# Kernel tuning notes

Hardware: AMD Instinct MI355X
Metric: run time of the kernel (lower is better)

The kernel has to match this reference:

```python
import jax, jax.numpy as jnp
import numpy as np

# dims
V = 50000      # vocab_size
DW = 50        # word_embed_size
DP = 5         # pos_embed_size
D = DW + 2 * DP  # input_size = 60
OC = 230       # out_c
NREL = 53      # n_rel
POSV = 61      # 2*pos_limit + 1
LIMIT = 30     # piecewise split threshold
G, B, L = 1000, 8, 120  # n_bags, bag_size, sentence length


def setup_inputs() -> dict:
    key = jax.random.key(0)
    ks = jax.random.split(key, 11)
    f32 = jnp.float32
    words = jax.random.randint(ks[0], (G, B, L), 0, V, dtype=jnp.int32)
    pos = jax.random.randint(ks[1], (G, B, L, 2), 0, POSV, dtype=jnp.int32)
    # pretrained-style word embeddings + position embeddings
    w2v = jax.random.normal(ks[2], (V, DW), f32) * 0.1
    pos1_emb = jax.random.normal(ks[3], (POSV, DP), f32) * 0.1
    pos2_emb = jax.random.normal(ks[4], (POSV, DP), f32) * 0.1
    con1 = float(np.sqrt(6.0 / ((DP + DW) * 3)))
    conv_w = jax.random.uniform(ks[5], (OC, 1, 3, D), f32, -con1, con1)  # OIHW
    conv_b0 = jax.random.uniform(ks[6], (1, OC), f32, -con1, con1)
    conv_b1 = jax.random.uniform(ks[7], (1, OC), f32, -con1, con1)
    conv_b2 = jax.random.uniform(ks[8], (1, OC), f32, -con1, con1)
    con = float(np.sqrt(6.0 / (OC + NREL)))
    r_embed = jax.random.uniform(ks[9], (NREL, 3 * OC), f32, -con, con)
    r_bias = jax.random.uniform(ks[10], (NREL,), f32, -con, con)
    return dict(words=words, pos=pos, w2v=w2v, pos1_emb=pos1_emb,
                pos2_emb=pos2_emb, conv_w=conv_w, conv_b0=conv_b0,
                conv_b1=conv_b1, conv_b2=conv_b2, r_embed=r_embed,
                r_bias=r_bias)


def reference(words, pos, w2v, pos1_emb, pos2_emb, conv_w,
              conv_b0, conv_b1, conv_b2, r_embed, r_bias):
    g, bag, ln = words.shape
    n = g * bag
    w = words.reshape(n, ln)
    p = pos.reshape(n, ln, 2)
    # embedding lookups -> [N, L, D]
    x = jnp.concatenate([w2v[w], pos1_emb[p[..., 0]], pos2_emb[p[..., 1]]], axis=-1)
    # Conv1d(1, OC, (3, D), padding=(1, 0)) over [N,1,L,D] -> [N,OC,L]
    feat = jax.lax.conv_general_dilated(
        x[:, None, :, :], conv_w, window_strides=(1, 1),
        padding=((1, 1), (0, 0)),
        dimension_numbers=('NCHW', 'OIHW', 'NCHW'))[..., 0]
    # piecewise masks from position ids
    p1 = (p[..., 0] >= LIMIT).astype(feat.dtype)  # [N, L]
    p2 = (p[..., 1] >= LIMIT).astype(feat.dtype)
    left = p1 * p2
    right = (1.0 - p1) * (1.0 - p2)
    mid = 1.0 - left - right

    def pool(mask, bias):  # masked max over sequence + per-piece bias
        return jnp.max(feat * mask[:, None, :], axis=-1) + bias  # [N, OC]

    f = jnp.concatenate([pool(left, conv_b0), pool(mid, conv_b1),
                         pool(right, conv_b2)], axis=-1)  # [N, 3*OC]
    f = jnp.tanh(f)
    # eval mode: dropout identity, logits scaled by 0.5 before bias
    logits = (f @ r_embed.T) * 0.5 + r_bias  # [N, NREL]
    logp = jax.nn.log_softmax(logits, axis=-1).reshape(g, bag, NREL)
    # eval mode: max over sentences in each bag
    return jnp.max(logp, axis=1)  # [G, NREL]
```

## Files before the change

### kernel.cpp

```cpp
#include <hip/hip_runtime.h>
#include <hip/hip_bf16.h>
#include <math.h>

typedef __bf16 bf16;
typedef __bf16 bf16x4 __attribute__((ext_vector_type(4)));
typedef __bf16 bf16x8 __attribute__((ext_vector_type(8)));
typedef float f32x4 __attribute__((ext_vector_type(4)));

#define OCC 230
#define NRELS 53
#define W2V48_OFF 0
#define WTAIL_OFF 2400000
#define PCAT_OFF  2500000
#define REMBB_OFF 2559552
#define CONVB_OFF 2608704
#define FLWS_OFF  2657862

union FragU { bf16x8 v8; bf16x4 v4[2]; bf16 e[8]; };

__global__ void pcnn_prep(const float* __restrict__ w2v, const float* __restrict__ p1e,
                          const float* __restrict__ p2e, const float* __restrict__ remb,
                          const float* __restrict__ convw, bf16* __restrict__ wsb) {
  const int i = blockIdx.x * 256 + threadIdx.x;
  if (i < 300000) {
    const int w = i / 6, c = i - 6 * w;
    const float2* s = reinterpret_cast<const float2*>(w2v + w * 50 + c * 8);
    const float2 f0 = s[0], f1 = s[1], f2 = s[2], f3 = s[3];
    bf16x8 v = {(bf16)f0.x, (bf16)f0.y, (bf16)f1.x, (bf16)f1.y,
                (bf16)f2.x, (bf16)f2.y, (bf16)f3.x, (bf16)f3.y};
    *reinterpret_cast<bf16x8*>(wsb + W2V48_OFF + w * 48 + c * 8) = v;
    return;
  }
  int e = i - 300000;
  if (e < 50000) {
    const float2 f = *reinterpret_cast<const float2*>(w2v + e * 50 + 48);
    wsb[WTAIL_OFF + 2 * e]     = (bf16)f.x;
    wsb[WTAIL_OFF + 2 * e + 1] = (bf16)f.y;
    return;
  }
  e -= 50000;
  if (e < 7442) {
    const int row = e >> 1, h = e & 1;
    const int v1 = row / 61, v2 = row - v1 * 61;
    bf16x8 v;
    if (h == 0) {
      v[0] = (bf16)p1e[v1 * 5 + 0]; v[1] = (bf16)p1e[v1 * 5 + 1];
      v[2] = (bf16)p1e[v1 * 5 + 2]; v[3] = (bf16)p1e[v1 * 5 + 3];
      v[4] = (bf16)p1e[v1 * 5 + 4]; v[5] = (bf16)p2e[v2 * 5 + 0];
      v[6] = (bf16)0.f; v[7] = (bf16)0.f;
    } else {
      v[0] = (bf16)p2e[v2 * 5 + 1]; v[1] = (bf16)p2e[v2 * 5 + 2];
      v[2] = (bf16)p2e[v2 * 5 + 3]; v[3] = (bf16)p2e[v2 * 5 + 4];
      v[4] = (bf16)0.f; v[5] = (bf16)0.f; v[6] = (bf16)0.f; v[7] = (bf16)0.f;
    }
    *reinterpret_cast<bf16x8*>(wsb + PCAT_OFF + row * 16 + h * 8) = v;
    return;
  }
  e -= 7442;
  if (e < 6144) {
    const int r = e / 96, c0 = (e - r * 96) * 8;
    bf16x8 v;
#pragma unroll
    for (int j = 0; j < 8; ++j) {
      const int cc = c0 + j, p = cc >> 8, oc = cc & 255;
      v[j] = (r < NRELS && oc < OCC) ? (bf16)remb[r * 690 + p * OCC + oc] : (bf16)0.f;
    }
    *reinterpret_cast<bf16x8*>(wsb + REMBB_OFF + r * 768 + c0) = v;
    return;
  }
  e -= 6144;
  if (e < 6144) {
    const int oc = e / 24, k0 = (e - oc * 24) * 8;
    bf16x8 v;
#pragma unroll
    for (int j = 0; j < 8; ++j) {
      const int k = k0 + j;
      v[j] = (oc < OCC && k < 180) ? (bf16)convw[oc * 180 + k] : (bf16)0.f;
    }
    *reinterpret_cast<bf16x8*>(wsb + CONVB_OFF + oc * 192 + k0) = v;
  }
}

#define XE 7352

__global__ __launch_bounds__(256, 3)
void pcnn_conv(const int* __restrict__ words, const int* __restrict__ posi,
               const float* __restrict__ cb0, const float* __restrict__ cb1,
               const float* __restrict__ cb2, const bf16* __restrict__ wsb,
               bf16* __restrict__ flws)
{
  __shared__ __align__(16) bf16 xlds[XE];
  __shared__ int widx[120];

  const int t = threadIdx.x;
  const int bid = blockIdx.x;
  const int ns = bid >> 1;
  const int ochalf = bid & 1;
  const int wv = t >> 6, lane = t & 63, g = lane >> 4, cl = lane & 15;

  if (t < 120) {
    const int w = words[ns * 120 + t];
    const int2 pp = *reinterpret_cast<const int2*>(posi + ns * 240 + 2 * t);
    const bool b0 = pp.x >= 30, b1 = pp.y >= 30;
    const int pc = (b0 && b1) ? 0 : ((!b0 && !b1) ? 2 : 1);
    widx[t] = w | ((pp.x * 61 + pp.y) << 16) | (pc << 28);
  }
  if (t < 16) {
    const int r = (t >> 3) ? 121 : 0;
    const int gr = t & 7;
    const int eo = r * 60 + ((gr < 7) ? gr * 8 : 52);
    *reinterpret_cast<int2*>(&xlds[eo])     = int2{0, 0};
    *reinterpret_cast<int2*>(&xlds[eo + 4]) = int2{0, 0};
  }

  FragU Bf[2][6];
  {
    const bf16* cwb = wsb + CONVB_OFF;
#pragma unroll
    for (int nt = 0; nt < 2; ++nt) {
      const int oc = ochalf * 128 + wv * 32 + nt * 16 + cl;
#pragma unroll
      for (int ks = 0; ks < 6; ++ks)
        Bf[nt][ks].v8 = *reinterpret_cast<const bf16x8*>(cwb + oc * 192 + ks * 32 + g * 8);
    }
  }
  __syncthreads();

#pragma unroll
  for (int k = 0; k < 4; ++k) {
    const int gi = t + k * 256;
    if (gi < 960) {
      const int lr = 1 + (gi >> 3), gr = gi & 7;
      const int wi = widx[lr - 1];
      const int word = wi & 0xFFFF;
      const int pidx = (wi >> 16) & 0xFFF;
      if (gr < 6) {
        const int4 v = *reinterpret_cast<const int4*>(wsb + W2V48_OFF + word * 48 + gr * 8);
        bf16* d = &xlds[lr * 60 + gr * 8];
        *reinterpret_cast<int2*>(d)     = int2{v.x, v.y};
        *reinterpret_cast<int2*>(d + 4) = int2{v.z, v.w};
      } else if (gr == 6) {
        const int wt = *(reinterpret_cast<const int*>(wsb + WTAIL_OFF) + word);
        const int4 pc4 = *reinterpret_cast<const int4*>(wsb + PCAT_OFF + pidx * 16);
        bf16* d = &xlds[lr * 60 + 48];
        *reinterpret_cast<int2*>(d)     = int2{wt, pc4.x};
        *reinterpret_cast<int2*>(d + 4) = int2{pc4.y, pc4.z};
      } else {
        const int2 v = *reinterpret_cast<const int2*>(wsb + PCAT_OFF + pidx * 16 + 8);
        *reinterpret_cast<int2*>(&xlds[lr * 60 + 56]) = v;
      }
    }
  }
  __syncthreads();

  int mrow[8];
#pragma unroll
  for (int mt = 0; mt < 8; ++mt) {
    const int m = mt * 16 + cl;
    mrow[mt] = (m < 120 ? m : 119) * 60;
  }

  f32x4 acc[8][2];
  const f32x4 z4 = {0.f, 0.f, 0.f, 0.f};
#pragma unroll
  for (int mt = 0; mt < 8; ++mt) { acc[mt][0] = z4; acc[mt][1] = z4; }

#pragma unroll
  for (int ks = 0; ks < 6; ++ks) {
    const int ko = ks * 32 + g * 8;
#pragma unroll
    for (int mt = 0; mt < 8; ++mt) {
      FragU a;
      a.v4[0] = *reinterpret_cast<const bf16x4*>(&xlds[mrow[mt] + ko]);
      a.v4[1] = *reinterpret_cast<const bf16x4*>(&xlds[mrow[mt] + ko + 4]);
#pragma unroll
      for (int nt = 0; nt < 2; ++nt)
        acc[mt][nt] = __builtin_amdgcn_mfma_f32_16x16x32_bf16(
            a.v8, Bf[nt][ks].v8, acc[mt][nt], 0, 0, 0);
    }
  }

  float pool[2][3];
#pragma unroll
  for (int nt = 0; nt < 2; ++nt) { pool[nt][0] = pool[nt][1] = pool[nt][2] = -INFINITY; }
#pragma unroll
  for (int mt = 0; mt < 8; ++mt) {
    const int l0 = mt * 16 + g * 4;
    if (l0 < 120) {
      const int4 pv = *reinterpret_cast<const int4*>(&widx[l0]);
      const int pcs[4] = {(int)((unsigned)pv.x >> 28), (int)((unsigned)pv.y >> 28),
                          (int)((unsigned)pv.z >> 28), (int)((unsigned)pv.w >> 28)};
#pragma unroll
      for (int r = 0; r < 4; ++r) {
        const int p = pcs[r];
#pragma unroll
        for (int nt = 0; nt < 2; ++nt) {
          const float v = acc[mt][nt][r];
          pool[nt][0] = fmaxf(pool[nt][0], p == 0 ? v : 0.0f);
          pool[nt][1] = fmaxf(pool[nt][1], p == 1 ? v : 0.0f);
          pool[nt][2] = fmaxf(pool[nt][2], p == 2 ? v : 0.0f);
        }
      }
    }
  }
#pragma unroll
  for (int nt = 0; nt < 2; ++nt)
#pragma unroll
    for (int p = 0; p < 3; ++p) {
      float x = pool[nt][p];
      x = fmaxf(x, __shfl_xor(x, 16));
      x = fmaxf(x, __shfl_xor(x, 32));
      pool[nt][p] = x;
    }

  if (g == 0) {
#pragma unroll
    for (int nt = 0; nt < 2; ++nt) {
      const int ocg = ochalf * 128 + wv * 32 + nt * 16 + cl;
      if (ocg < OCC) {
        const float b0v = cb0[ocg], b1v = cb1[ocg], b2v = cb2[ocg];
        bf16* fr = flws + ns * 768;
        fr[ocg]       = (bf16)tanhf(pool[nt][0] + b0v);
        fr[256 + ocg] = (bf16)tanhf(pool[nt][1] + b1v);
        fr[512 + ocg] = (bf16)tanhf(pool[nt][2] + b2v);
      }
    }
  }
}

__global__ __launch_bounds__(256)
void pcnn_logits(const bf16* __restrict__ wsb, const bf16* __restrict__ flws,
                 const float* __restrict__ rbias, float* __restrict__ out)
{
  __shared__ __align__(16) bf16 fl_lds[6144];
  __shared__ float logits_l[8][64];

  const int t = threadIdx.x;
  const int bag = blockIdx.x;
  const int wv = t >> 6, lane = t & 63, g = lane >> 4, cl = lane & 15;

#pragma unroll
  for (int j = 0; j < 3; ++j) {
    const bf16* src = flws + bag * 6144 + (j * 256 + t) * 8;
    bf16* dst = &fl_lds[(j * 256 + wv * 64) * 8];
    __builtin_amdgcn_global_load_lds(
        (const __attribute__((address_space(1))) void*)src,
        (__attribute__((address_space(3))) void*)dst, 16, 0, 0);
  }
  asm volatile("s_waitcnt vmcnt(0)" ::: "memory");
  __syncthreads();

  f32x4 lac = {0.f, 0.f, 0.f, 0.f};
  const bf16* brow = wsb + REMBB_OFF + (wv * 16 + cl) * 768 + g * 8;
  const bf16x8 zf = {(bf16)0.f, (bf16)0.f, (bf16)0.f, (bf16)0.f,
                     (bf16)0.f, (bf16)0.f, (bf16)0.f, (bf16)0.f};
#pragma unroll
  for (int ks = 0; ks < 24; ++ks) {
    const bf16x8 afr = (cl < 8)
        ? *reinterpret_cast<const bf16x8*>(&fl_lds[cl * 768 + ks * 32 + g * 8]) : zf;
    const bf16x8 bfr = *reinterpret_cast<const bf16x8*>(brow + ks * 32);
    lac = __builtin_amdgcn_mfma_f32_16x16x32_bf16(afr, bfr, lac, 0, 0, 0);
  }
  if (g < 2) {
    const int rel = wv * 16 + cl;
    const float bias = (rel < NRELS) ? rbias[rel] : 0.0f;
#pragma unroll
    for (int r = 0; r < 4; ++r)
      logits_l[g * 4 + r][rel] = lac[r] * 0.5f + bias;
  }
  __syncthreads();

#pragma unroll
  for (int rep = 0; rep < 2; ++rep) {
    const int s = wv + rep * 4;
    const float x = (lane < NRELS) ? logits_l[s][lane] : -INFINITY;
    float m = x;
#pragma unroll
    for (int off = 32; off; off >>= 1) m = fmaxf(m, __shfl_xor(m, off));
    const float e = (lane < NRELS) ? __expf(x - m) : 0.0f;
    float sm = e;
#pragma unroll
    for (int off = 32; off; off >>= 1) sm += __shfl_xor(sm, off);
    if (lane < NRELS) logits_l[s][lane] = x - m - __logf(sm);
  }
  __syncthreads();

  if (t < NRELS) {
    float m = logits_l[0][t];
#pragma unroll
    for (int s2 = 1; s2 < 8; ++s2) m = fmaxf(m, logits_l[s2][t]);
    out[bag * NRELS + t] = m;
  }
}

extern "C" void kernel_launch(void* const* d_in, const int* in_sizes, int n_in,
                              void* d_out, int out_size, void* d_ws, size_t ws_size,
                              hipStream_t stream) {
  const int* words  = (const int*)d_in[0];
  const int* posi   = (const int*)d_in[1];
  const float* w2v  = (const float*)d_in[2];
  const float* p1e  = (const float*)d_in[3];
  const float* p2e  = (const float*)d_in[4];
  const float* cw   = (const float*)d_in[5];
  const float* cb0  = (const float*)d_in[6];
  const float* cb1  = (const float*)d_in[7];
  const float* cb2  = (const float*)d_in[8];
  const float* remb = (const float*)d_in[9];
  const float* rbias= (const float*)d_in[10];
  bf16* wsb = (bf16*)d_ws;
  bf16* flws = wsb + FLWS_OFF;
  float* out = (float*)d_out;

  pcnn_prep<<<1445, 256, 0, stream>>>(w2v, p1e, p2e, remb, cw, wsb);
  pcnn_conv<<<16000, 256, 0, stream>>>(words, posi, cb0, cb1, cb2, wsb, flws);
  pcnn_logits<<<1000, 256, 0, stream>>>(wsb, flws, rbias, out);
}
```

Measured before the change: 313.7 us.

## Double-buffer gathered embeddings with async global-to-LDS loads over four sentences per block

The conv kernel now runs 512-thread blocks that cover all 256 output channels and loop over four sentences. The embedding rows of the next sentence are gathered into a second LDS buffer with global_load_lds while the current one is being computed. The LDS rows are padded to a stride of 64 and XOR-swizzled, and the conv weights are re-laid out per tap, so each A fragment is one 16-byte read without bank conflicts. Conv weights and biases are loaded once per block instead of once per sentence. The trade-offs are fewer blocks (2000 instead of 16000), a larger per-block LDS footprint, and a full-buffer zeroing pass at the start of each block.

Result: slower. 342.7 us (+9.3%).

```diff
diff --git a/kernel.cpp b/kernel.cpp
--- a/kernel.cpp
+++ b/kernel.cpp
@@ -14,7 +14,7 @@
 #define PCAT_OFF  2500000
 #define REMBB_OFF 2559552
 #define CONVB_OFF 2608704
-#define FLWS_OFF  2657862
+#define FLWS_OFF  2657864
 
 union FragU { bf16x8 v8; bf16x4 v4[2]; bf16 e[8]; };
 
@@ -74,43 +74,44 @@
     bf16x8 v;
 #pragma unroll
     for (int j = 0; j < 8; ++j) {
-      const int k = k0 + j;
-      v[j] = (oc < OCC && k < 180) ? (bf16)convw[oc * 180 + k] : (bf16)0.f;
+      const int kp = k0 + j, tap = kp >> 6, d = kp & 63;
+      v[j] = (oc < OCC && d < 60) ? (bf16)convw[oc * 180 + tap * 60 + d] : (bf16)0.f;
     }
     *reinterpret_cast<bf16x8*>(wsb + CONVB_OFF + oc * 192 + k0) = v;
   }
 }
 
-#define XE 7352
-
-__global__ __launch_bounds__(256, 3)
+#define XROWS 122
+#define XSTR 64
+#define XBUFE (XROWS * XSTR)
+
+__global__ __launch_bounds__(512, 4)
 void pcnn_conv(const int* __restrict__ words, const int* __restrict__ posi,
                const float* __restrict__ cb0, const float* __restrict__ cb1,
                const float* __restrict__ cb2, const bf16* __restrict__ wsb,
                bf16* __restrict__ flws)
 {
-  __shared__ __align__(16) bf16 xlds[XE];
-  __shared__ int widx[120];
+  __shared__ __align__(16) bf16 xb[2][XBUFE];
+  __shared__ int widx[480];
 
   const int t = threadIdx.x;
-  const int bid = blockIdx.x;
-  const int ns = bid >> 1;
-  const int ochalf = bid & 1;
+  const int sb = blockIdx.x * 4;
   const int wv = t >> 6, lane = t & 63, g = lane >> 4, cl = lane & 15;
 
-  if (t < 120) {
-    const int w = words[ns * 120 + t];
-    const int2 pp = *reinterpret_cast<const int2*>(posi + ns * 240 + 2 * t);
+  if (t < 480) {
+    const int w = words[sb * 120 + t];
+    const int2 pp = *reinterpret_cast<const int2*>(posi + sb * 240 + 2 * t);
     const bool b0 = pp.x >= 30, b1 = pp.y >= 30;
     const int pc = (b0 && b1) ? 0 : ((!b0 && !b1) ? 2 : 1);
     widx[t] = w | ((pp.x * 61 + pp.y) << 16) | (pc << 28);
   }
-  if (t < 16) {
-    const int r = (t >> 3) ? 121 : 0;
-    const int gr = t & 7;
-    const int eo = r * 60 + ((gr < 7) ? gr * 8 : 52);
-    *reinterpret_cast<int2*>(&xlds[eo])     = int2{0, 0};
-    *reinterpret_cast<int2*>(&xlds[eo + 4]) = int2{0, 0};
+  {
+    int4* z = reinterpret_cast<int4*>(&xb[0][0]);
+#pragma unroll
+    for (int i = 0; i < 4; ++i) {
+      const int idx = t + i * 512;
+      if (idx < 2 * XBUFE / 8) z[idx] = int4{0, 0, 0, 0};
+    }
   }
 
   FragU Bf[2][6];
@@ -118,113 +119,140 @@
     const bf16* cwb = wsb + CONVB_OFF;
 #pragma unroll
     for (int nt = 0; nt < 2; ++nt) {
-      const int oc = ochalf * 128 + wv * 32 + nt * 16 + cl;
+      const int oc = wv * 32 + nt * 16 + cl;
 #pragma unroll
       for (int ks = 0; ks < 6; ++ks)
         Bf[nt][ks].v8 = *reinterpret_cast<const bf16x8*>(cwb + oc * 192 + ks * 32 + g * 8);
     }
   }
-  __syncthreads();
-
-#pragma unroll
-  for (int k = 0; k < 4; ++k) {
-    const int gi = t + k * 256;
-    if (gi < 960) {
-      const int lr = 1 + (gi >> 3), gr = gi & 7;
-      const int wi = widx[lr - 1];
+  float bias[2][3];
+#pragma unroll
+  for (int nt = 0; nt < 2; ++nt) {
+    const int ocg = wv * 32 + nt * 16 + cl;
+    const int occ = (ocg < OCC) ? ocg : 0;
+    bias[nt][0] = cb0[occ]; bias[nt][1] = cb1[occ]; bias[nt][2] = cb2[occ];
+  }
+
+  __syncthreads();
+
+  auto issue_gather = [&](int s, int nb) {
+    const int* wr = &widx[s * 120];
+#pragma unroll
+    for (int i = 0; i < 2; ++i) {
+      const int slotb = wv * 128 + i * 64;
+      const int slot = slotb + lane;
+      const int row = slot >> 3;
+      const int c16 = (slot & 7) ^ (row & 7);
+      bf16* dst = &xb[nb][slotb * 8];
+      if (row >= 1 && row <= 120 && c16 < 6) {
+        const int word = wr[row - 1] & 0xFFFF;
+        const bf16* src = wsb + W2V48_OFF + word * 48 + c16 * 8;
+        __builtin_amdgcn_global_load_lds(
+            (const __attribute__((address_space(1))) void*)src,
+            (__attribute__((address_space(3))) void*)dst, 16, 0, 0);
+      }
+    }
+  };
+  auto stage_tail = [&](int s, int nb) {
+    if (t < 120) {
+      const int wi = widx[s * 120 + t];
       const int word = wi & 0xFFFF;
       const int pidx = (wi >> 16) & 0xFFF;
-      if (gr < 6) {
-        const int4 v = *reinterpret_cast<const int4*>(wsb + W2V48_OFF + word * 48 + gr * 8);
-        bf16* d = &xlds[lr * 60 + gr * 8];
-        *reinterpret_cast<int2*>(d)     = int2{v.x, v.y};
-        *reinterpret_cast<int2*>(d + 4) = int2{v.z, v.w};
-      } else if (gr == 6) {
-        const int wt = *(reinterpret_cast<const int*>(wsb + WTAIL_OFF) + word);
-        const int4 pc4 = *reinterpret_cast<const int4*>(wsb + PCAT_OFF + pidx * 16);
-        bf16* d = &xlds[lr * 60 + 48];
-        *reinterpret_cast<int2*>(d)     = int2{wt, pc4.x};
-        *reinterpret_cast<int2*>(d + 4) = int2{pc4.y, pc4.z};
-      } else {
-        const int2 v = *reinterpret_cast<const int2*>(wsb + PCAT_OFF + pidx * 16 + 8);
-        *reinterpret_cast<int2*>(&xlds[lr * 60 + 56]) = v;
-      }
-    }
-  }
-  __syncthreads();
-
-  int mrow[8];
+      const int row = t + 1;
+      const int wt = *(reinterpret_cast<const int*>(wsb + WTAIL_OFF) + word);
+      const int4 pcA = *reinterpret_cast<const int4*>(wsb + PCAT_OFF + pidx * 16);
+      const int4 pcB = *reinterpret_cast<const int4*>(wsb + PCAT_OFF + pidx * 16 + 8);
+      const int sw6 = 6 ^ (row & 7), sw7 = 7 ^ (row & 7);
+      *reinterpret_cast<int4*>(&xb[nb][row * XSTR + sw6 * 8]) = int4{wt, pcA.x, pcA.y, pcA.z};
+      *reinterpret_cast<int4*>(&xb[nb][row * XSTR + sw7 * 8]) = pcB;
+    }
+  };
+
+  issue_gather(0, 0);
+  stage_tail(0, 0);
+  asm volatile("s_waitcnt vmcnt(0)" ::: "memory");
+  __syncthreads();
+
+  int mrowT[8];
 #pragma unroll
   for (int mt = 0; mt < 8; ++mt) {
     const int m = mt * 16 + cl;
-    mrow[mt] = (m < 120 ? m : 119) * 60;
-  }
-
-  f32x4 acc[8][2];
-  const f32x4 z4 = {0.f, 0.f, 0.f, 0.f};
-#pragma unroll
-  for (int mt = 0; mt < 8; ++mt) { acc[mt][0] = z4; acc[mt][1] = z4; }
-
-#pragma unroll
-  for (int ks = 0; ks < 6; ++ks) {
-    const int ko = ks * 32 + g * 8;
+    mrowT[mt] = (m < 120 ? m : 119) * XSTR;
+  }
+
+  for (int s = 0; s < 4; ++s) {
+    const int nb = s & 1;
+    if (s < 3) { issue_gather(s + 1, nb ^ 1); stage_tail(s + 1, nb ^ 1); }
+
+    f32x4 acc[8][2];
+    const f32x4 z4 = {0.f, 0.f, 0.f, 0.f};
+#pragma unroll
+    for (int mt = 0; mt < 8; ++mt) { acc[mt][0] = z4; acc[mt][1] = z4; }
+
+#pragma unroll
+    for (int ks = 0; ks < 6; ++ks) {
+      const int kp = ks * 32 + g * 8;
+      const int tap = kp >> 6;
+      const int d8 = (kp >> 3) & 7;
+      const int sw = tap * XSTR + ((d8 ^ ((cl + tap) & 7)) << 3);
+#pragma unroll
+      for (int mt = 0; mt < 8; ++mt) {
+        FragU a;
+        a.v8 = *reinterpret_cast<const bf16x8*>(&xb[nb][mrowT[mt] + sw]);
+#pragma unroll
+        for (int nt = 0; nt < 2; ++nt)
+          acc[mt][nt] = __builtin_amdgcn_mfma_f32_16x16x32_bf16(
+              a.v8, Bf[nt][ks].v8, acc[mt][nt], 0, 0, 0);
+      }
+    }
+
+    float pool[2][3];
+#pragma unroll
+    for (int nt = 0; nt < 2; ++nt) { pool[nt][0] = pool[nt][1] = pool[nt][2] = -INFINITY; }
 #pragma unroll
     for (int mt = 0; mt < 8; ++mt) {
-      FragU a;
-      a.v4[0] = *reinterpret_cast<const bf16x4*>(&xlds[mrow[mt] + ko]);
-      a.v4[1] = *reinterpret_cast<const bf16x4*>(&xlds[mrow[mt] + ko + 4]);
-#pragma unroll
-      for (int nt = 0; nt < 2; ++nt)
-        acc[mt][nt] = __builtin_amdgcn_mfma_f32_16x16x32_bf16(
-            a.v8, Bf[nt][ks].v8, acc[mt][nt], 0, 0, 0);
-    }
-  }
-
-  float pool[2][3];
-#pragma unroll
-  for (int nt = 0; nt < 2; ++nt) { pool[nt][0] = pool[nt][1] = pool[nt][2] = -INFINITY; }
-#pragma unroll
-  for (int mt = 0; mt < 8; ++mt) {
-    const int l0 = mt * 16 + g * 4;
-    if (l0 < 120) {
-      const int4 pv = *reinterpret_cast<const int4*>(&widx[l0]);
-      const int pcs[4] = {(int)((unsigned)pv.x >> 28), (int)((unsigned)pv.y >> 28),
-                          (int)((unsigned)pv.z >> 28), (int)((unsigned)pv.w >> 28)};
-#pragma unroll
-      for (int r = 0; r < 4; ++r) {
-        const int p = pcs[r];
-#pragma unroll
-        for (int nt = 0; nt < 2; ++nt) {
-          const float v = acc[mt][nt][r];
-          pool[nt][0] = fmaxf(pool[nt][0], p == 0 ? v : 0.0f);
-          pool[nt][1] = fmaxf(pool[nt][1], p == 1 ? v : 0.0f);
-          pool[nt][2] = fmaxf(pool[nt][2], p == 2 ? v : 0.0f);
+      const int l0 = mt * 16 + g * 4;
+      if (l0 < 120) {
+        const int4 pv = *reinterpret_cast<const int4*>(&widx[s * 120 + l0]);
+        const int pcs[4] = {(int)((unsigned)pv.x >> 28), (int)((unsigned)pv.y >> 28),
+                            (int)((unsigned)pv.z >> 28), (int)((unsigned)pv.w >> 28)};
+#pragma unroll
+        for (int r = 0; r < 4; ++r) {
+          const int p = pcs[r];
+#pragma unroll
+          for (int nt = 0; nt < 2; ++nt) {
+            const float v = acc[mt][nt][r];
+            pool[nt][0] = fmaxf(pool[nt][0], p == 0 ? v : 0.0f);
+            pool[nt][1] = fmaxf(pool[nt][1], p == 1 ? v : 0.0f);
+            pool[nt][2] = fmaxf(pool[nt][2], p == 2 ? v : 0.0f);
+          }
         }
       }
     }
-  }
-#pragma unroll
-  for (int nt = 0; nt < 2; ++nt)
-#pragma unroll
-    for (int p = 0; p < 3; ++p) {
-      float x = pool[nt][p];
-      x = fmaxf(x, __shfl_xor(x, 16));
-      x = fmaxf(x, __shfl_xor(x, 32));
-      pool[nt][p] = x;
-    }
-
-  if (g == 0) {
-#pragma unroll
-    for (int nt = 0; nt < 2; ++nt) {
-      const int ocg = ochalf * 128 + wv * 32 + nt * 16 + cl;
-      if (ocg < OCC) {
-        const float b0v = cb0[ocg], b1v = cb1[ocg], b2v = cb2[ocg];
-        bf16* fr = flws + ns * 768;
-        fr[ocg]       = (bf16)tanhf(pool[nt][0] + b0v);
-        fr[256 + ocg] = (bf16)tanhf(pool[nt][1] + b1v);
-        fr[512 + ocg] = (bf16)tanhf(pool[nt][2] + b2v);
-      }
-    }
+#pragma unroll
+    for (int nt = 0; nt < 2; ++nt)
+#pragma unroll
+      for (int p = 0; p < 3; ++p) {
+        float x = pool[nt][p];
+        x = fmaxf(x, __shfl_xor(x, 16));
+        x = fmaxf(x, __shfl_xor(x, 32));
+        pool[nt][p] = x;
+      }
+    if (g == 0) {
+#pragma unroll
+      for (int nt = 0; nt < 2; ++nt) {
+        const int ocg = wv * 32 + nt * 16 + cl;
+        if (ocg < OCC) {
+          bf16* fr = flws + (sb + s) * 768;
+          fr[ocg]       = (bf16)tanhf(pool[nt][0] + bias[nt][0]);
+          fr[256 + ocg] = (bf16)tanhf(pool[nt][1] + bias[nt][1]);
+          fr[512 + ocg] = (bf16)tanhf(pool[nt][2] + bias[nt][2]);
+        }
+      }
+    }
+
+    asm volatile("s_waitcnt vmcnt(0)" ::: "memory");
+    __syncthreads();
   }
 }
 
@@ -312,6 +340,6 @@
   float* out = (float*)d_out;
 
   pcnn_prep<<<1445, 256, 0, stream>>>(w2v, p1e, p2e, remb, cw, wsb);
-  pcnn_conv<<<16000, 256, 0, stream>>>(words, posi, cb0, cb1, cb2, wsb, flws);
+  pcnn_conv<<<2000, 512, 0, stream>>>(words, posi, cb0, cb1, cb2, wsb, flws);
   pcnn_logits<<<1000, 256, 0, stream>>>(wsb, flws, rbias, out);
 }
```
